# Performance work log

Measured on AMD Instinct MI355X. Metric: run time of the kernel, lower is better.

## Reference

```python
import jax, jax.numpy as jnp
import numpy as np

B, K, D, V = 8192, 32, 128, 2048
WEIGHT, SIGMA, NDCG_K = 0.15, 1.0, 10
N = K + 1


def _to_hyperboloid(x):
    # lift spatial coords onto Lorentz hyperboloid: x0 = sqrt(1 + ||x||^2)
    t = jnp.sqrt(1.0 + jnp.sum(x * x, axis=-1, keepdims=True))
    return jnp.concatenate([t, x], axis=-1)


def _lorentz_dist(u, v):
    # d(u,v) = arccosh(-<u,v>_L), <u,v>_L = -u0*v0 + u[1:].v[1:]
    inner = -u[..., 0] * v[..., 0] + jnp.sum(u[..., 1:] * v[..., 1:], axis=-1)
    return jnp.arccosh(jnp.maximum(-inner, 1.0 + 1e-7))


def setup_inputs() -> dict:
    key = jax.random.key(0)
    k = jax.random.split(key, 7)
    anchor_emb = _to_hyperboloid(jax.random.normal(k[0], (B, D), dtype=jnp.float32))
    positive_emb = _to_hyperboloid(jax.random.normal(k[1], (B, D), dtype=jnp.float32))
    negative_embs = _to_hyperboloid(jax.random.normal(k[2], (B * K, D), dtype=jnp.float32))
    tree_distances = jax.random.uniform(k[3], (V, V), dtype=jnp.float32) * 10.0
    anchor_idx = jax.random.randint(k[4], (B,), 0, V, dtype=jnp.int32)
    pos_idx = jax.random.randint(k[5], (B,), 0, V, dtype=jnp.int32)
    neg_idx = jax.random.randint(k[6], (B, K), 0, V, dtype=jnp.int32)
    return {"anchor_emb": anchor_emb, "positive_emb": positive_emb,
            "negative_embs": negative_embs, "tree_distances": tree_distances,
            "anchor_idx": anchor_idx, "pos_idx": pos_idx, "neg_idx": neg_idx}


def _lambdarank(anchor_emb, positive_emb, negative_embs, tree_distances,
                anchor_idx, pos_idx, neg_idx):
    neg = negative_embs.reshape(B, K, -1)
    pos_dist = _lorentz_dist(anchor_emb, positive_emb)            # (B,)
    neg_dists = _lorentz_dist(anchor_emb[:, None, :], neg)        # (B,K)
    d = jnp.concatenate([pos_dist[:, None], neg_dists], axis=1)   # (B,N)

    pos_t = tree_distances[anchor_idx, pos_idx]                   # (B,)
    neg_t = tree_distances[anchor_idx[:, None], neg_idx]          # (B,K)
    t = jnp.concatenate([pos_t[:, None], neg_t], axis=1)          # (B,N)
    max_t = jnp.max(t, axis=1, keepdims=True)
    rel = (max_t - t + 1e-6) / (max_t + 1e-6)                     # (B,N)

    k_top = min(NDCG_K, N)
    # 1-based rank of each item under ascending-distance sort (piecewise const)
    ranks = jnp.argsort(jnp.argsort(d, axis=1), axis=1) + 1       # (B,N)
    disc = jnp.where(ranks <= k_top,
                     1.0 / jnp.log2(ranks.astype(jnp.float32) + 1.0), 0.0)
    ideal = -jnp.sort(-rel, axis=1)[:, :k_top]                    # (B,k)
    log_pos = jnp.log2(jnp.arange(2, k_top + 2, dtype=jnp.float32))
    idcg = jnp.sum(ideal / log_pos, axis=1)                       # (B,)

    # closed-form |delta NDCG| of swapping items i,j in the ranking:
    # |(rel_i - rel_j) * (disc_i - disc_j)| / IDCG
    drel = rel[:, :, None] - rel[:, None, :]                      # (B,N,N)
    ddisc = disc[:, :, None] - disc[:, None, :]
    inv_idcg = jnp.where(idcg > 0, 1.0 / idcg, 0.0)[:, None, None]
    delta = jnp.abs(drel * ddisc) * inv_idcg

    # lambda_ij = sign(rel_i-rel_j) * delta * sigmoid(sign * sigma * (d_j - d_i))
    S = jnp.sign(drel)
    dd = d[:, None, :] - d[:, :, None]                            # d_j - d_i
    lam = S * delta * jax.nn.sigmoid(S * SIGMA * dd)
    # loss = sum_{i<j} lam_ij*(d_i-d_j); antisymmetric -> 0.5 * full sum
    loss_b = 0.5 * jnp.sum(lam * (-dd), axis=(1, 2))              # (B,)
    return WEIGHT * jnp.mean(loss_b)


def reference(anchor_emb, positive_emb, negative_embs, tree_distances,
              anchor_idx, pos_idx, neg_idx):
    return _lambdarank(anchor_emb, positive_emb, negative_embs, tree_distances,
                       anchor_idx, pos_idx, neg_idx)
```

## Files before the change

### kernel.cpp

```cpp
#include <hip/hip_runtime.h>
#include <math.h>

#define BB 8192
#define KK 32
#define DD 129
#define VV 2048
#define NN 33
#define TOPK 10
#define WPB 4

__device__ __forceinline__ float fast_rcp(float x) { return __builtin_amdgcn_rcpf(x); }
__device__ __forceinline__ float dot4(float4 a, float4 b) {
    return fmaf(a.x, b.x, fmaf(a.y, b.y, fmaf(a.z, b.z, a.w * b.w)));
}

__global__ __launch_bounds__(256) void lr_fused(
    const float* __restrict__ anchor,
    const float* __restrict__ positive,
    const float* __restrict__ neg,
    const float* __restrict__ tree,
    const int* __restrict__ a_idx,
    const int* __restrict__ p_idx,
    const int* __restrict__ n_idx,
    float* __restrict__ partial)
{
    __shared__ float  st_[WPB][NN];
    __shared__ float  sx_[WPB][NN];
    __shared__ float  sd_[WPB][NN];
    __shared__ float4 sitem[WPB][NN];

    const int t    = threadIdx.x;
    const int wave = t >> 6;
    const int lane = t & 63;
    const int g    = lane >> 4;
    const int subl = lane & 15;
    const int b    = blockIdx.x * WPB + wave;

    const int ai  = a_idx[b];
    const int col = (lane == 0) ? p_idx[b]
                                : n_idx[(size_t)b * KK + ((lane < NN ? lane : KK) - 1)];
    const float tg = tree[(size_t)ai * VV + col];
    if (lane < NN) st_[wave][lane] = tg;

    const float* ab = anchor   + (size_t)b * DD;
    const float* pb = positive + (size_t)b * DD;
    const float* nb = neg      + (size_t)b * (KK * DD);

    float4 aq0 = *(const float4*)(ab + 4 * subl);
    float4 aq1 = *(const float4*)(ab + 64 + 4 * subl);
    const float a128 = ab[128];

    const float* rp[9];
    #pragma unroll
    for (int r = 0; r < 9; ++r) {
        int row = 4 * r + g;
        if (row > KK) row = KK;
        rp[r] = (row == 0) ? pb : (nb + (size_t)(row - 1) * DD);
    }
    float4 v0[9], v1[9];
    float  t128[9];
    #pragma unroll
    for (int r = 0; r < 9; ++r) {
        v0[r]   = *(const float4*)(rp[r] + 4 * subl);
        v1[r]   = *(const float4*)(rp[r] + 64 + 4 * subl);
        t128[r] = rp[r][128];
    }

    #pragma unroll
    for (int r = 0; r < 9; ++r) {
        float s = dot4(aq0, v0[r]) + dot4(aq1, v1[r]);
        s += __shfl_xor(s, 8, 64);
        s += __shfl_xor(s, 4, 64);
        s += __shfl_xor(s, 2, 64);
        s += __shfl_xor(s, 1, 64);
        int row = 4 * r + g;
        if (subl == 0 && row < NN) {
            float full = s + a128 * t128[r];
            sx_[wave][row] = fmaxf(fmaf(2.0f * aq0.x, v0[r].x, -full), 1.0f + 1e-07f);
        }
    }

    float dlane = 0.0f;
    if (lane < NN) {
        float x = sx_[wave][lane];
        dlane = __logf(x + sqrtf(x * x - 1.0f));
        sd_[wave][lane] = dlane;
    }

    if (lane < NN) {
        float maxt = st_[wave][0];
        #pragma unroll
        for (int j = 1; j < NN; ++j) maxt = fmaxf(maxt, st_[wave][j]);
        float rel = (maxt - tg + 1e-06f) * fast_rcp(maxt + 1e-06f);

        int cnt = 0;
        #pragma unroll
        for (int j = 0; j < NN; ++j) {
            float dj = sd_[wave][j];
            cnt += (int)((dj < dlane) | ((dj == dlane) & (j < lane)));
        }
        float disc = (cnt + 1 <= TOPK) ? fast_rcp(log2f((float)(cnt + 2))) : 0.0f;
        sitem[wave][lane] = make_float4(dlane, rel, disc, 0.0f);
    }

    float c = 0.0f;
    if (lane < NN) {
        float ri = sitem[wave][lane].y;
        int pos = 0;
        #pragma unroll
        for (int j = 0; j < NN; ++j) {
            float rj = sitem[wave][j].y;
            pos += (int)((rj > ri) | ((rj == ri) & (j < lane)));
        }
        if (pos < TOPK) c = ri * fast_rcp(log2f((float)(pos + 2)));
    }
    #pragma unroll
    for (int off = 32; off > 0; off >>= 1) c += __shfl_xor(c, off, 64);
    const float inv = (c > 0.0f) ? fast_rcp(c) : 0.0f;

    float acc = 0.0f;
    #pragma unroll
    for (int it = 0; it < 9; ++it) {
        int p = it * 64 + lane;
        float vmask = (p < 528) ? 1.0f : 0.0f;
        int pc = (p < 528) ? p : 527;
        int j = (int)((1.0f + sqrtf((float)(8 * pc + 1))) * 0.5f);
        int tj = (j * (j - 1)) >> 1;
        if (tj > pc) { --j; tj = (j * (j - 1)) >> 1; }
        int i = pc - tj;
        float4 Ii = sitem[wave][i];
        float4 Ij = sitem[wave][j];
        float dd    = Ij.x - Ii.x;
        float drel  = Ii.y - Ij.y;
        float ddisc = Ii.z - Ij.z;
        float t1  = drel * fabsf(ddisc) * (inv * vmask);
        float e   = __expf(-dd);
        float num = (drel >= 0.0f) ? 1.0f : e;
        acc = fmaf(t1 * num * fast_rcp(1.0f + e), -dd, acc);
    }
    #pragma unroll
    for (int off = 32; off > 0; off >>= 1) acc += __shfl_xor(acc, off, 64);
    if (lane == 0) partial[b] = acc;
}

__global__ __launch_bounds__(256) void lr_reduce(
    const float* __restrict__ partial, float* __restrict__ out)
{
    __shared__ float swave[4];
    const float4* p4 = (const float4*)partial;
    float acc = 0.0f;
    #pragma unroll
    for (int c = 0; c < (BB / 4) / 256; ++c) {
        float4 v = p4[c * 256 + threadIdx.x];
        acc += (v.x + v.y) + (v.z + v.w);
    }
    #pragma unroll
    for (int off = 32; off > 0; off >>= 1) acc += __shfl_xor(acc, off, 64);
    if ((threadIdx.x & 63) == 0) swave[threadIdx.x >> 6] = acc;
    __syncthreads();
    if (threadIdx.x == 0)
        out[0] = (swave[0] + swave[1] + swave[2] + swave[3]) * (0.15f / (float)BB);
}

extern "C" void kernel_launch(void* const* d_in, const int* in_sizes, int n_in,
                              void* d_out, int out_size, void* d_ws, size_t ws_size,
                              hipStream_t stream)
{
    const float* anchor   = (const float*)d_in[0];
    const float* positive = (const float*)d_in[1];
    const float* neg      = (const float*)d_in[2];
    const float* tree     = (const float*)d_in[3];
    const int*   a_idx    = (const int*)d_in[4];
    const int*   p_idx    = (const int*)d_in[5];
    const int*   n_idx    = (const int*)d_in[6];
    float* partial = (float*)d_ws;

    lr_fused<<<BB / WPB, 256, 0, stream>>>(anchor, positive, neg, tree,
                                           a_idx, p_idx, n_idx, partial);
    lr_reduce<<<1, 256, 0, stream>>>(partial, (float*)d_out);
}
```

Before: 225.6 us.

## Split distance computation into separate wide-block kernel before ranking

Moves the Lorentz inner-product computation out of the fused kernel into a new kernel with one 1024-thread block per batch row, each wave handling about two rows using scalar coalesced loads and full-wave reductions. Results go through a global workspace buffer that the ranking kernel then reads. The aim is more memory-level parallelism and fewer registers for the bandwidth-bound embedding reads. In exchange it adds a kernel launch, a global round trip for the intermediate values, and many threads that sit idle (most waves only do two dot products).

```diff
diff --git a/kernel.cpp b/kernel.cpp
--- a/kernel.cpp
+++ b/kernel.cpp
@@ -10,14 +10,68 @@
 #define WPB 4
 
 __device__ __forceinline__ float fast_rcp(float x) { return __builtin_amdgcn_rcpf(x); }
-__device__ __forceinline__ float dot4(float4 a, float4 b) {
-    return fmaf(a.x, b.x, fmaf(a.y, b.y, fmaf(a.z, b.z, a.w * b.w)));
-}
 
-__global__ __launch_bounds__(256) void lr_fused(
+__global__ __launch_bounds__(1024) void lr_dist(
     const float* __restrict__ anchor,
     const float* __restrict__ positive,
     const float* __restrict__ neg,
+    float* __restrict__ xout)
+{
+    const int b    = blockIdx.x;
+    const int wave = threadIdx.x >> 6;
+    const int lane = threadIdx.x & 63;
+
+    const float* ab = anchor   + (size_t)b * DD;
+    const float* pb = positive + (size_t)b * DD;
+    const float* nb = neg      + (size_t)b * (KK * DD);
+
+    const int row0 = wave;
+    const int row1 = wave + 16;
+    const float* r0 = (row0 == 0) ? pb : (nb + (size_t)(row0 - 1) * DD);
+    const float* r1 = nb + (size_t)(row1 - 1) * DD;
+
+    const float a_lo = ab[lane];
+    const float a_hi = ab[64 + lane];
+    const float a128 = ab[128];
+    const float v0_lo = r0[lane], v0_hi = r0[64 + lane], v0_128 = r0[128];
+    const float v1_lo = r1[lane], v1_hi = r1[64 + lane], v1_128 = r1[128];
+
+    {
+        float s = fmaf(a_lo, v0_lo, a_hi * v0_hi);
+        #pragma unroll
+        for (int off = 32; off > 0; off >>= 1) s += __shfl_xor(s, off, 64);
+        if (lane == 0) {
+            float full = s + a128 * v0_128;
+            float x = fmaxf(fmaf(2.0f * a_lo, v0_lo, -full), 1.0f + 1e-07f);
+            xout[(size_t)b * NN + row0] = x;
+        }
+    }
+    {
+        float s = fmaf(a_lo, v1_lo, a_hi * v1_hi);
+        #pragma unroll
+        for (int off = 32; off > 0; off >>= 1) s += __shfl_xor(s, off, 64);
+        if (lane == 0) {
+            float full = s + a128 * v1_128;
+            float x = fmaxf(fmaf(2.0f * a_lo, v1_lo, -full), 1.0f + 1e-07f);
+            xout[(size_t)b * NN + row1] = x;
+        }
+    }
+    if (wave == 0) {
+        const float* r2 = nb + (size_t)(KK - 1) * DD;
+        float v2_lo = r2[lane], v2_hi = r2[64 + lane], v2_128 = r2[128];
+        float s = fmaf(a_lo, v2_lo, a_hi * v2_hi);
+        #pragma unroll
+        for (int off = 32; off > 0; off >>= 1) s += __shfl_xor(s, off, 64);
+        if (lane == 0) {
+            float full = s + a128 * v2_128;
+            float x = fmaxf(fmaf(2.0f * a_lo, v2_lo, -full), 1.0f + 1e-07f);
+            xout[(size_t)b * NN + KK] = x;
+        }
+    }
+}
+
+__global__ __launch_bounds__(256) void lr_rank(
+    const float* __restrict__ xin,
     const float* __restrict__ tree,
     const int* __restrict__ a_idx,
     const int* __restrict__ p_idx,
@@ -25,15 +79,12 @@
     float* __restrict__ partial)
 {
     __shared__ float  st_[WPB][NN];
-    __shared__ float  sx_[WPB][NN];
     __shared__ float  sd_[WPB][NN];
     __shared__ float4 sitem[WPB][NN];
 
     const int t    = threadIdx.x;
     const int wave = t >> 6;
     const int lane = t & 63;
-    const int g    = lane >> 4;
-    const int subl = lane & 15;
     const int b    = blockIdx.x * WPB + wave;
 
     const int ai  = a_idx[b];
@@ -42,47 +93,9 @@
     const float tg = tree[(size_t)ai * VV + col];
     if (lane < NN) st_[wave][lane] = tg;
 
-    const float* ab = anchor   + (size_t)b * DD;
-    const float* pb = positive + (size_t)b * DD;
-    const float* nb = neg      + (size_t)b * (KK * DD);
-
-    float4 aq0 = *(const float4*)(ab + 4 * subl);
-    float4 aq1 = *(const float4*)(ab + 64 + 4 * subl);
-    const float a128 = ab[128];
-
-    const float* rp[9];
-    #pragma unroll
-    for (int r = 0; r < 9; ++r) {
-        int row = 4 * r + g;
-        if (row > KK) row = KK;
-        rp[r] = (row == 0) ? pb : (nb + (size_t)(row - 1) * DD);
-    }
-    float4 v0[9], v1[9];
-    float  t128[9];
-    #pragma unroll
-    for (int r = 0; r < 9; ++r) {
-        v0[r]   = *(const float4*)(rp[r] + 4 * subl);
-        v1[r]   = *(const float4*)(rp[r] + 64 + 4 * subl);
-        t128[r] = rp[r][128];
-    }
-
-    #pragma unroll
-    for (int r = 0; r < 9; ++r) {
-        float s = dot4(aq0, v0[r]) + dot4(aq1, v1[r]);
-        s += __shfl_xor(s, 8, 64);
-        s += __shfl_xor(s, 4, 64);
-        s += __shfl_xor(s, 2, 64);
-        s += __shfl_xor(s, 1, 64);
-        int row = 4 * r + g;
-        if (subl == 0 && row < NN) {
-            float full = s + a128 * t128[r];
-            sx_[wave][row] = fmaxf(fmaf(2.0f * aq0.x, v0[r].x, -full), 1.0f + 1e-07f);
-        }
-    }
-
     float dlane = 0.0f;
     if (lane < NN) {
-        float x = sx_[wave][lane];
+        float x = xin[(size_t)b * NN + lane];
         dlane = __logf(x + sqrtf(x * x - 1.0f));
         sd_[wave][lane] = dlane;
     }
@@ -173,9 +186,11 @@
     const int*   a_idx    = (const int*)d_in[4];
     const int*   p_idx    = (const int*)d_in[5];
     const int*   n_idx    = (const int*)d_in[6];
-    float* partial = (float*)d_ws;
 
-    lr_fused<<<BB / WPB, 256, 0, stream>>>(anchor, positive, neg, tree,
-                                           a_idx, p_idx, n_idx, partial);
+    float* xbuf    = (float*)d_ws;
+    float* partial = (float*)d_ws + (size_t)BB * NN;
+
+    lr_dist<<<BB, 1024, 0, stream>>>(anchor, positive, neg, xbuf);
+    lr_rank<<<BB / WPB, 256, 0, stream>>>(xbuf, tree, a_idx, p_idx, n_idx, partial);
     lr_reduce<<<1, 256, 0, stream>>>(partial, (float*)d_out);
 }
```

New measurement: 231.2 us. 1.02x slower.
